# Kernel tuning notes

Hardware: AMD Instinct MI355X
Metric: run time of the kernel (lower is better)

The kernel has to match this reference:

```python
import jax, jax.numpy as jnp
import numpy as np

N_NODES = 10000
N_EDGES = 320000


def _graph_conv(x, W, b, src, dst, n):
    # DGL GraphConv, norm='both': D_out^{-1/2} on src side, aggregate, D_in^{-1/2} on dst side,
    # then linear + bias. Degrees clamped at 1 (allow_zero_in_degree=True).
    ones = jnp.ones(src.shape[0], dtype=x.dtype)
    deg_out = jnp.clip(jax.ops.segment_sum(ones, src, num_segments=n), 1.0)
    deg_in = jnp.clip(jax.ops.segment_sum(ones, dst, num_segments=n), 1.0)
    h = x * jax.lax.rsqrt(deg_out)[:, None]          # [n, f] scaled source feats
    agg = jax.ops.segment_sum(h[src], dst, num_segments=n)  # gather + scatter-add
    agg = agg * jax.lax.rsqrt(deg_in)[:, None]
    return agg @ W + b


def setup_inputs() -> dict:
    key = jax.random.key(0)
    ks = jax.random.split(key, 8)
    in_dim, h1, h2 = 512, 256, 128
    features = jax.random.normal(ks[0], (N_NODES, in_dim), dtype=jnp.float32)
    src = jax.random.randint(ks[1], (N_EDGES,), 0, N_NODES)
    dst = jax.random.randint(ks[2], (N_EDGES,), 0, N_NODES)
    noise = jax.random.normal(ks[3], (N_NODES, h2), dtype=jnp.float32)
    W1 = jax.random.normal(ks[4], (in_dim, h1), dtype=jnp.float32) / np.sqrt(in_dim)
    b1 = jnp.zeros((h1,), dtype=jnp.float32)
    W2 = jax.random.normal(ks[5], (h1, h2), dtype=jnp.float32) / np.sqrt(h1)
    b2 = jnp.zeros((h2,), dtype=jnp.float32)
    W3 = jax.random.normal(ks[6], (h1, h2), dtype=jnp.float32) / np.sqrt(h1)
    b3 = jnp.zeros((h2,), dtype=jnp.float32)
    return {"features": features, "src": src, "dst": dst, "noise": noise,
            "W1": W1, "b1": b1, "W2": W2, "b2": b2, "W3": W3, "b3": b3}


def reference(features, src, dst, noise, W1, b1, W2, b2, W3, b3):
    n = features.shape[0]
    h = jax.nn.relu(_graph_conv(features, W1, b1, src, dst, n))
    mean = _graph_conv(h, W2, b2, src, dst, n)
    log_std = _graph_conv(h, W3, b3, src, dst, n)
    z = mean + noise * jnp.exp(log_std)              # reparameterization
    adj_rec = jax.nn.sigmoid(z @ z.T)                # inner-product decoder [N, N]
    return adj_rec
```

## Files before the change

kernel.cpp:

```cpp
#include <hip/hip_runtime.h>
#include <hip/hip_fp16.h>


#define NN 10000
#define NE 320000
#define FD 512
#define H1 256
#define H2 128

typedef _Float16 half8 __attribute__((ext_vector_type(8)));
typedef _Float16 half4 __attribute__((ext_vector_type(4)));
typedef float f32x4 __attribute__((ext_vector_type(4)));

__device__ __forceinline__ void acc4(float4& a, const float4 v) {
    a.x += v.x; a.y += v.y; a.z += v.z; a.w += v.w;
}

__global__ void k_zero2(int* __restrict__ a, int* __restrict__ b, int n) {
    int i = blockIdx.x * blockDim.x + threadIdx.x;
    if (i < n) { a[i] = 0; b[i] = 0; }
}

__global__ void k_count(const int* __restrict__ src, const int* __restrict__ dst,
                        int* __restrict__ co, int* __restrict__ ci) {
    int e = blockIdx.x * blockDim.x + threadIdx.x;
    if (e < NE) {
        atomicAdd(&co[src[e]], 1);
        atomicAdd(&ci[dst[e]], 1);
    }
}

__global__ __launch_bounds__(1024) void k_scan(const int* __restrict__ ci, const int* __restrict__ co,
                                               int* __restrict__ row_ptr, int* __restrict__ cursor,
                                               float* __restrict__ rs_in, float* __restrict__ rs_out) {
    __shared__ int sm[1024];
    int tid = threadIdx.x;
    const int CH = (NN + 1023) / 1024;
    int base = tid * CH;
    int local[CH];
    int s = 0;
    #pragma unroll
    for (int i = 0; i < CH; ++i) {
        int idx = base + i;
        local[i] = s;
        if (idx < NN) s += ci[idx];
    }
    sm[tid] = s;
    __syncthreads();
    for (int off = 1; off < 1024; off <<= 1) {
        int v = (tid >= off) ? sm[tid - off] : 0;
        __syncthreads();
        sm[tid] += v;
        __syncthreads();
    }
    int excl = sm[tid] - s;
    #pragma unroll
    for (int i = 0; i < CH; ++i) {
        int idx = base + i;
        if (idx < NN) row_ptr[idx] = excl + local[i];
    }
    if (tid == 1023) row_ptr[NN] = sm[1023];
    for (int i = tid; i < NN; i += 1024) {
        int a = ci[i], b = co[i];
        rs_in[i]  = rsqrtf((float)(a > 1 ? a : 1));
        rs_out[i] = rsqrtf((float)(b > 1 ? b : 1));
        cursor[i] = 0;
    }
}

__global__ void k_bucket(const int* __restrict__ src, const int* __restrict__ dst,
                         const int* __restrict__ row_ptr, int* __restrict__ cursor,
                         int* __restrict__ esrc) {
    int e = blockIdx.x * blockDim.x + threadIdx.x;
    if (e < NE) {
        int d = dst[e];
        int p = row_ptr[d] + atomicAdd(&cursor[d], 1);
        esrc[p] = src[e];
    }
}

__global__ void k_castW(const float* __restrict__ W1, const float* __restrict__ W2,
                        const float* __restrict__ W3, const float* __restrict__ b2,
                        const float* __restrict__ b3,
                        _Float16* __restrict__ W1Th, _Float16* __restrict__ W1Tl,
                        _Float16* __restrict__ WcTh, _Float16* __restrict__ WcTl,
                        float* __restrict__ biasC) {
    int idx = blockIdx.x * blockDim.x + threadIdx.x;
    if (idx < FD * H1) {
        int k = idx >> 8, n = idx & 255;
        float v = W1[idx];
        _Float16 h = (_Float16)v;
        W1Th[n * FD + k] = h;
        W1Tl[n * FD + k] = (_Float16)(v - (float)h);
    } else if (idx < FD * H1 + H1 * H1) {
        int j = idx - FD * H1;
        int k = j >> 8, n = j & 255;
        float v = (n < H2) ? W2[k * H2 + n] : W3[k * H2 + (n - H2)];
        _Float16 h = (_Float16)v;
        WcTh[n * H1 + k] = h;
        WcTl[n * H1 + k] = (_Float16)(v - (float)h);
        if (k == 0) biasC[n] = (n < H2) ? b2[n] : b3[n - H2];
    }
}

template <int K>
__global__ __launch_bounds__(256) void k_gemm16(
    const float* __restrict__ A, const float* __restrict__ ascale,
    const _Float16* __restrict__ BTh, const _Float16* __restrict__ BTl,
    const float* __restrict__ bias, float* __restrict__ C, int M) {
    __shared__ __align__(16) _Float16 Ahs[64][72];
    __shared__ __align__(16) _Float16 Als[64][72];
    __shared__ __align__(16) _Float16 Bhs[64][72];
    __shared__ __align__(16) _Float16 Bls[64][72];
    int tid = threadIdx.x;
    int lane = tid & 63;
    int w = tid >> 6;
    int wr = (w >> 1) * 32, wc = (w & 1) * 32;
    int bm = blockIdx.x * 64, bn = blockIdx.y * 64;
    f32x4 acc[2][2] = {};
    for (int k0 = 0; k0 < K; k0 += 64) {
        __syncthreads();
        #pragma unroll
        for (int i = 0; i < 4; ++i) {
            int lin = i * 256 + tid;
            int r = lin >> 4, c = lin & 15;
            int gr = bm + r;
            float4 v = {0.f, 0.f, 0.f, 0.f};
            float s = 1.0f;
            if (gr < M) {
                v = *(const float4*)(A + (size_t)gr * K + k0 + c * 4);
                if (ascale) s = ascale[gr];
            }
            v.x *= s; v.y *= s; v.z *= s; v.w *= s;
            half4 hh = { (_Float16)v.x, (_Float16)v.y, (_Float16)v.z, (_Float16)v.w };
            half4 ll = { (_Float16)(v.x - (float)hh.x), (_Float16)(v.y - (float)hh.y),
                         (_Float16)(v.z - (float)hh.z), (_Float16)(v.w - (float)hh.w) };
            *(half4*)&Ahs[r][c * 4] = hh;
            *(half4*)&Als[r][c * 4] = ll;
        }
        #pragma unroll
        for (int i = 0; i < 2; ++i) {
            int lin = i * 256 + tid;
            int r = lin >> 3, c = lin & 7;
            *(int4*)&Bhs[r][c * 8] = *(const int4*)(BTh + (size_t)(bn + r) * K + k0 + c * 8);
            *(int4*)&Bls[r][c * 8] = *(const int4*)(BTl + (size_t)(bn + r) * K + k0 + c * 8);
        }
        __syncthreads();
        #pragma unroll
        for (int ks = 0; ks < 2; ++ks) {
            int kof = ks * 32 + ((lane >> 4) << 3);
            half8 ah[2], al[2], bh[2], bl[2];
            #pragma unroll
            for (int f = 0; f < 2; ++f) {
                ah[f] = *(const half8*)&Ahs[wr + f * 16 + (lane & 15)][kof];
                al[f] = *(const half8*)&Als[wr + f * 16 + (lane & 15)][kof];
                bh[f] = *(const half8*)&Bhs[wc + f * 16 + (lane & 15)][kof];
                bl[f] = *(const half8*)&Bls[wc + f * 16 + (lane & 15)][kof];
            }
            #pragma unroll
            for (int i = 0; i < 2; ++i)
                #pragma unroll
                for (int j = 0; j < 2; ++j) {
                    acc[i][j] = __builtin_amdgcn_mfma_f32_16x16x32_f16(ah[i], bh[j], acc[i][j], 0, 0, 0);
                    acc[i][j] = __builtin_amdgcn_mfma_f32_16x16x32_f16(ah[i], bl[j], acc[i][j], 0, 0, 0);
                    acc[i][j] = __builtin_amdgcn_mfma_f32_16x16x32_f16(al[i], bh[j], acc[i][j], 0, 0, 0);
                }
        }
    }
    int quad = lane >> 4, c16 = lane & 15;
    #pragma unroll
    for (int i = 0; i < 2; ++i) {
        int row0 = bm + wr + i * 16 + quad * 4;
        #pragma unroll
        for (int j = 0; j < 2; ++j) {
            int col = bn + wc + j * 16 + c16;
            float bb = bias ? bias[col] : 0.0f;
            #pragma unroll
            for (int r = 0; r < 4; ++r) {
                int row = row0 + r;
                if (row < M) C[(size_t)row * H1 + col] = acc[i][j][r] + bb;
            }
        }
    }
}

template <bool FIRST>
__global__ __launch_bounds__(256) void k_agg(const float* __restrict__ in, float* __restrict__ out,
                                             const int* __restrict__ esrc, const int* __restrict__ row_ptr,
                                             const float* __restrict__ rs_in, const float* __restrict__ rs_out,
                                             const float* __restrict__ bias) {
    int node = (blockIdx.x * blockDim.x + threadIdx.x) >> 6;
    int lane = threadIdx.x & 63;
    if (node >= NN) return;
    int beg = row_ptr[node], end = row_ptr[node + 1];
    float4 acc = {0.f, 0.f, 0.f, 0.f};
    int e = beg;
    for (; e + 4 <= end; e += 4) {
        int s0 = esrc[e + 0], s1 = esrc[e + 1], s2 = esrc[e + 2], s3 = esrc[e + 3];
        float4 v0 = ((const float4*)(in + (size_t)s0 * H1))[lane];
        float4 v1 = ((const float4*)(in + (size_t)s1 * H1))[lane];
        float4 v2 = ((const float4*)(in + (size_t)s2 * H1))[lane];
        float4 v3 = ((const float4*)(in + (size_t)s3 * H1))[lane];
        acc4(acc, v0); acc4(acc, v1); acc4(acc, v2); acc4(acc, v3);
    }
    for (; e < end; ++e) {
        float4 v0 = ((const float4*)(in + (size_t)esrc[e] * H1))[lane];
        acc4(acc, v0);
    }
    float si = rs_in[node];
    float4 r;
    r.x = acc.x * si; r.y = acc.y * si; r.z = acc.z * si; r.w = acc.w * si;
    if (FIRST) {
        float4 bb = ((const float4*)bias)[lane];
        float so = rs_out[node];
        r.x = fmaxf(r.x + bb.x, 0.f) * so;
        r.y = fmaxf(r.y + bb.y, 0.f) * so;
        r.z = fmaxf(r.z + bb.z, 0.f) * so;
        r.w = fmaxf(r.w + bb.w, 0.f) * so;
    }
    ((float4*)(out + (size_t)node * H1))[lane] = r;
}

__global__ void k_z(const float* __restrict__ ml, const float* __restrict__ noise,
                    _Float16* __restrict__ z) {
    int i = blockIdx.x * blockDim.x + threadIdx.x;
    if (i < NN * H2) {
        int r = i >> 7, c = i & 127;
        float mean = ml[(size_t)r * 256 + c];
        float ls   = ml[(size_t)r * 256 + 128 + c];
        z[i] = (_Float16)(mean + noise[i] * __expf(ls));
    }
}

__global__ __launch_bounds__(256) void k_decoder(const _Float16* __restrict__ Z, float* __restrict__ out) {
    __shared__ __align__(16) _Float16 As[128][72];
    __shared__ __align__(16) _Float16 Bs[128][72];
    int tid = threadIdx.x;
    int lane = tid & 63;
    int w = tid >> 6;
    int wrow = (w >> 1) * 64;
    int wcol = (w & 1) * 64;
    int rowBase = blockIdx.y * 128;
    int colBase = blockIdx.x * 128;
    f32x4 acc[4][4] = {};
    for (int s = 0; s < 2; ++s) {
        __syncthreads();
        #pragma unroll
        for (int i = 0; i < 4; ++i) {
            int lin = i * 256 + tid;
            int r = lin >> 3, c = lin & 7;
            int4 v = {0, 0, 0, 0};
            int gr = rowBase + r;
            if (gr < NN) v = *(const int4*)(Z + (size_t)gr * H2 + s * 64 + c * 8);
            *(int4*)&As[r][c * 8] = v;
            int4 u = {0, 0, 0, 0};
            int gc = colBase + r;
            if (gc < NN) u = *(const int4*)(Z + (size_t)gc * H2 + s * 64 + c * 8);
            *(int4*)&Bs[r][c * 8] = u;
        }
        __syncthreads();
        #pragma unroll
        for (int kk = 0; kk < 2; ++kk) {
            int kof = kk * 32 + ((lane >> 4) << 3);
            half8 a[4], b[4];
            #pragma unroll
            for (int f = 0; f < 4; ++f) a[f] = *(const half8*)&As[wrow + f * 16 + (lane & 15)][kof];
            #pragma unroll
            for (int f = 0; f < 4; ++f) b[f] = *(const half8*)&Bs[wcol + f * 16 + (lane & 15)][kof];
            #pragma unroll
            for (int i = 0; i < 4; ++i)
                #pragma unroll
                for (int j = 0; j < 4; ++j)
                    acc[i][j] = __builtin_amdgcn_mfma_f32_16x16x32_f16(a[i], b[j], acc[i][j], 0, 0, 0);
        }
    }
    #pragma unroll
    for (int i = 0; i < 4; ++i) {
        int row0 = rowBase + wrow + i * 16 + ((lane >> 4) << 2);
        #pragma unroll
        for (int j = 0; j < 4; ++j) {
            int col = colBase + wcol + j * 16 + (lane & 15);
            if (col < NN) {
                #pragma unroll
                for (int r = 0; r < 4; ++r) {
                    int row = row0 + r;
                    if (row < NN) {
                        float x = acc[i][j][r];
                        float sg = 1.0f / (1.0f + __expf(-x));
                        __builtin_nontemporal_store(sg, out + (size_t)row * NN + col);
                    }
                }
            }
        }
    }
}

extern "C" void kernel_launch(void* const* d_in, const int* in_sizes, int n_in,
                              void* d_out, int out_size, void* d_ws, size_t ws_size,
                              hipStream_t stream) {
    const float* features = (const float*)d_in[0];
    const int*   src      = (const int*)d_in[1];
    const int*   dst      = (const int*)d_in[2];
    const float* noise    = (const float*)d_in[3];
    const float* W1 = (const float*)d_in[4];
    const float* b1 = (const float*)d_in[5];
    const float* W2 = (const float*)d_in[6];
    const float* b2 = (const float*)d_in[7];
    const float* W3 = (const float*)d_in[8];
    const float* b3 = (const float*)d_in[9];
    float* out = (float*)d_out;
    (void)in_sizes; (void)n_in; (void)out_size; (void)ws_size;

    char* ws = (char*)d_ws;
    size_t off = 0;
    auto alloc = [&](size_t bytes) -> void* {
        void* p = ws + off;
        off += (bytes + 255) & ~(size_t)255;
        return p;
    };
    int* degc_out = (int*)alloc(NN * sizeof(int));
    int* degc_in  = (int*)alloc(NN * sizeof(int));
    int* row_ptr  = (int*)alloc((NN + 1) * sizeof(int));
    int* cursor   = (int*)alloc(NN * sizeof(int));
    int* esrc     = (int*)alloc(NE * sizeof(int));
    float* rs_out = (float*)alloc(NN * sizeof(float));
    float* rs_in  = (float*)alloc(NN * sizeof(float));
    _Float16* W1Th = (_Float16*)alloc((size_t)H1 * FD * sizeof(_Float16));
    _Float16* W1Tl = (_Float16*)alloc((size_t)H1 * FD * sizeof(_Float16));
    _Float16* WcTh = (_Float16*)alloc((size_t)H1 * H1 * sizeof(_Float16));
    _Float16* WcTl = (_Float16*)alloc((size_t)H1 * H1 * sizeof(_Float16));
    float* biasC  = (float*)alloc(H1 * sizeof(float));
    float* bufA   = (float*)alloc((size_t)NN * H1 * sizeof(float));
    float* bufB   = (float*)alloc((size_t)NN * H1 * sizeof(float));
    _Float16* Zh  = (_Float16*)alloc((size_t)NN * H2 * sizeof(_Float16));

    k_zero2<<<(NN + 255) / 256, 256, 0, stream>>>(degc_out, degc_in, NN);
    k_count<<<(NE + 255) / 256, 256, 0, stream>>>(src, dst, degc_out, degc_in);
    k_scan<<<1, 1024, 0, stream>>>(degc_in, degc_out, row_ptr, cursor, rs_in, rs_out);
    k_bucket<<<(NE + 255) / 256, 256, 0, stream>>>(src, dst, row_ptr, cursor, esrc);
    k_castW<<<(FD * H1 + H1 * H1 + 255) / 256, 256, 0, stream>>>(
        W1, W2, W3, b2, b3, W1Th, W1Tl, WcTh, WcTl, biasC);

    k_gemm16<FD><<<dim3((NN + 63) / 64, H1 / 64), 256, 0, stream>>>(
        features, rs_out, W1Th, W1Tl, nullptr, bufA, NN);
    k_agg<true><<<NN / 4, 256, 0, stream>>>(bufA, bufB, esrc, row_ptr, rs_in, rs_out, b1);
    k_agg<false><<<NN / 4, 256, 0, stream>>>(bufB, bufA, esrc, row_ptr, rs_in, nullptr, nullptr);
    k_gemm16<H1><<<dim3((NN + 63) / 64, H1 / 64), 256, 0, stream>>>(
        bufA, nullptr, WcTh, WcTl, biasC, bufB, NN);
    k_z<<<(NN * H2 + 255) / 256, 256, 0, stream>>>(bufB, noise, Zh);
    k_decoder<<<dim3((NN + 127) / 128, (NN + 127) / 128), 256, 0, stream>>>(Zh, out);
}
```

Measured before the change: 660.7 us.

## Store intermediate features as fp16 and fuse reparameterization into second GEMM

The first GEMM output and the post-ReLU hidden features are now stored as fp16, so the two gather-heavy aggregation kernels read half the bytes per edge. The second GEMM is restructured to compute matching mean and log_std column tiles in one block and apply bias, exp and the noise combination in its epilogue. This removes the separate k_z kernel and the fp32 round trip of the combined output. Smaller tweaks fold the cursor zeroing into the zero kernel and use a hardware reciprocal in the sigmoid. The fp16 storage of intermediates adds rounding error relative to the previous split-fp16 fp32 path.

Result: faster. 625.6 us (-5.3%).

```diff
diff --git a/kernel.cpp b/kernel.cpp
--- a/kernel.cpp
+++ b/kernel.cpp
@@ -12,13 +12,9 @@
 typedef _Float16 half4 __attribute__((ext_vector_type(4)));
 typedef float f32x4 __attribute__((ext_vector_type(4)));
 
-__device__ __forceinline__ void acc4(float4& a, const float4 v) {
-    a.x += v.x; a.y += v.y; a.z += v.z; a.w += v.w;
-}
-
-__global__ void k_zero2(int* __restrict__ a, int* __restrict__ b, int n) {
+__global__ void k_zero3(int* __restrict__ a, int* __restrict__ b, int* __restrict__ c, int n) {
     int i = blockIdx.x * blockDim.x + threadIdx.x;
-    if (i < n) { a[i] = 0; b[i] = 0; }
+    if (i < n) { a[i] = 0; b[i] = 0; c[i] = 0; }
 }
 
 __global__ void k_count(const int* __restrict__ src, const int* __restrict__ dst,
@@ -31,7 +27,7 @@
 }
 
 __global__ __launch_bounds__(1024) void k_scan(const int* __restrict__ ci, const int* __restrict__ co,
-                                               int* __restrict__ row_ptr, int* __restrict__ cursor,
+                                               int* __restrict__ row_ptr,
                                                float* __restrict__ rs_in, float* __restrict__ rs_out) {
     __shared__ int sm[1024];
     int tid = threadIdx.x;
@@ -64,7 +60,6 @@
         int a = ci[i], b = co[i];
         rs_in[i]  = rsqrtf((float)(a > 1 ? a : 1));
         rs_out[i] = rsqrtf((float)(b > 1 ? b : 1));
-        cursor[i] = 0;
     }
 }
 
@@ -80,11 +75,9 @@
 }
 
 __global__ void k_castW(const float* __restrict__ W1, const float* __restrict__ W2,
-                        const float* __restrict__ W3, const float* __restrict__ b2,
-                        const float* __restrict__ b3,
+                        const float* __restrict__ W3,
                         _Float16* __restrict__ W1Th, _Float16* __restrict__ W1Tl,
-                        _Float16* __restrict__ WcTh, _Float16* __restrict__ WcTl,
-                        float* __restrict__ biasC) {
+                        _Float16* __restrict__ WcTh, _Float16* __restrict__ WcTl) {
     int idx = blockIdx.x * blockDim.x + threadIdx.x;
     if (idx < FD * H1) {
         int k = idx >> 8, n = idx & 255;
@@ -99,15 +92,14 @@
         _Float16 h = (_Float16)v;
         WcTh[n * H1 + k] = h;
         WcTl[n * H1 + k] = (_Float16)(v - (float)h);
-        if (k == 0) biasC[n] = (n < H2) ? b2[n] : b3[n - H2];
-    }
-}
-
-template <int K>
-__global__ __launch_bounds__(256) void k_gemm16(
+    }
+}
+
+__global__ __launch_bounds__(256) void k_gemm1(
     const float* __restrict__ A, const float* __restrict__ ascale,
     const _Float16* __restrict__ BTh, const _Float16* __restrict__ BTl,
-    const float* __restrict__ bias, float* __restrict__ C, int M) {
+    _Float16* __restrict__ C, int M) {
+    const int K = FD;
     __shared__ __align__(16) _Float16 Ahs[64][72];
     __shared__ __align__(16) _Float16 Als[64][72];
     __shared__ __align__(16) _Float16 Bhs[64][72];
@@ -129,12 +121,12 @@
             float s = 1.0f;
             if (gr < M) {
                 v = *(const float4*)(A + (size_t)gr * K + k0 + c * 4);
-                if (ascale) s = ascale[gr];
+                s = ascale[gr];
             }
             v.x *= s; v.y *= s; v.z *= s; v.w *= s;
             half4 hh = { (_Float16)v.x, (_Float16)v.y, (_Float16)v.z, (_Float16)v.w };
-            half4 ll = { (_Float16)(v.x - (float)hh.x), (_Float16)(v.y - (float)hh.y),
-                         (_Float16)(v.z - (float)hh.z), (_Float16)(v.w - (float)hh.w) };
+            half4 ll = { (_Float16)(v.x - (float)hh[0]), (_Float16)(v.y - (float)hh[1]),
+                         (_Float16)(v.z - (float)hh[2]), (_Float16)(v.w - (float)hh[3]) };
             *(half4*)&Ahs[r][c * 4] = hh;
             *(half4*)&Als[r][c * 4] = ll;
         }
@@ -174,18 +166,113 @@
         #pragma unroll
         for (int j = 0; j < 2; ++j) {
             int col = bn + wc + j * 16 + c16;
-            float bb = bias ? bias[col] : 0.0f;
             #pragma unroll
             for (int r = 0; r < 4; ++r) {
                 int row = row0 + r;
-                if (row < M) C[(size_t)row * H1 + col] = acc[i][j][r] + bb;
+                if (row < M) C[(size_t)row * H1 + col] = (_Float16)acc[i][j][r];
+            }
+        }
+    }
+}
+
+__global__ __launch_bounds__(256) void k_gemm2z(
+    const float* __restrict__ A,
+    const _Float16* __restrict__ BTh, const _Float16* __restrict__ BTl,
+    const float* __restrict__ b2, const float* __restrict__ b3,
+    const float* __restrict__ noise, _Float16* __restrict__ Zh, int M) {
+    const int K = H1;
+    __shared__ __align__(16) _Float16 Ahs[64][72];
+    __shared__ __align__(16) _Float16 Als[64][72];
+    __shared__ __align__(16) _Float16 Bmh[64][72];
+    __shared__ __align__(16) _Float16 Bml[64][72];
+    __shared__ __align__(16) _Float16 Blh[64][72];
+    __shared__ __align__(16) _Float16 Bll[64][72];
+    int tid = threadIdx.x;
+    int lane = tid & 63;
+    int w = tid >> 6;
+    int wr = (w >> 1) * 32, wc = (w & 1) * 32;
+    int bm = blockIdx.x * 64;
+    int c0 = blockIdx.y * 64;
+    f32x4 accm[2][2] = {};
+    f32x4 accl[2][2] = {};
+    for (int k0 = 0; k0 < K; k0 += 64) {
+        __syncthreads();
+        #pragma unroll
+        for (int i = 0; i < 4; ++i) {
+            int lin = i * 256 + tid;
+            int r = lin >> 4, c = lin & 15;
+            int gr = bm + r;
+            float4 v = {0.f, 0.f, 0.f, 0.f};
+            if (gr < M) v = *(const float4*)(A + (size_t)gr * K + k0 + c * 4);
+            half4 hh = { (_Float16)v.x, (_Float16)v.y, (_Float16)v.z, (_Float16)v.w };
+            half4 ll = { (_Float16)(v.x - (float)hh[0]), (_Float16)(v.y - (float)hh[1]),
+                         (_Float16)(v.z - (float)hh[2]), (_Float16)(v.w - (float)hh[3]) };
+            *(half4*)&Ahs[r][c * 4] = hh;
+            *(half4*)&Als[r][c * 4] = ll;
+        }
+        #pragma unroll
+        for (int i = 0; i < 2; ++i) {
+            int lin = i * 256 + tid;
+            int r = lin >> 3, c = lin & 7;
+            size_t rm = (size_t)(c0 + r) * K + k0 + c * 8;
+            size_t rl = (size_t)(128 + c0 + r) * K + k0 + c * 8;
+            *(int4*)&Bmh[r][c * 8] = *(const int4*)(BTh + rm);
+            *(int4*)&Bml[r][c * 8] = *(const int4*)(BTl + rm);
+            *(int4*)&Blh[r][c * 8] = *(const int4*)(BTh + rl);
+            *(int4*)&Bll[r][c * 8] = *(const int4*)(BTl + rl);
+        }
+        __syncthreads();
+        #pragma unroll
+        for (int ks = 0; ks < 2; ++ks) {
+            int kof = ks * 32 + ((lane >> 4) << 3);
+            half8 ah[2], al[2], mh[2], ml[2], lh[2], ll[2];
+            #pragma unroll
+            for (int f = 0; f < 2; ++f) {
+                ah[f] = *(const half8*)&Ahs[wr + f * 16 + (lane & 15)][kof];
+                al[f] = *(const half8*)&Als[wr + f * 16 + (lane & 15)][kof];
+                mh[f] = *(const half8*)&Bmh[wc + f * 16 + (lane & 15)][kof];
+                ml[f] = *(const half8*)&Bml[wc + f * 16 + (lane & 15)][kof];
+                lh[f] = *(const half8*)&Blh[wc + f * 16 + (lane & 15)][kof];
+                ll[f] = *(const half8*)&Bll[wc + f * 16 + (lane & 15)][kof];
+            }
+            #pragma unroll
+            for (int i = 0; i < 2; ++i)
+                #pragma unroll
+                for (int j = 0; j < 2; ++j) {
+                    accm[i][j] = __builtin_amdgcn_mfma_f32_16x16x32_f16(ah[i], mh[j], accm[i][j], 0, 0, 0);
+                    accm[i][j] = __builtin_amdgcn_mfma_f32_16x16x32_f16(ah[i], ml[j], accm[i][j], 0, 0, 0);
+                    accm[i][j] = __builtin_amdgcn_mfma_f32_16x16x32_f16(al[i], mh[j], accm[i][j], 0, 0, 0);
+                    accl[i][j] = __builtin_amdgcn_mfma_f32_16x16x32_f16(ah[i], lh[j], accl[i][j], 0, 0, 0);
+                    accl[i][j] = __builtin_amdgcn_mfma_f32_16x16x32_f16(ah[i], ll[j], accl[i][j], 0, 0, 0);
+                    accl[i][j] = __builtin_amdgcn_mfma_f32_16x16x32_f16(al[i], lh[j], accl[i][j], 0, 0, 0);
+                }
+        }
+    }
+    int quad = lane >> 4, c16 = lane & 15;
+    #pragma unroll
+    for (int i = 0; i < 2; ++i) {
+        int row0 = bm + wr + i * 16 + quad * 4;
+        #pragma unroll
+        for (int j = 0; j < 2; ++j) {
+            int c = c0 + wc + j * 16 + c16;
+            float bm_ = b2[c], bl_ = b3[c];
+            #pragma unroll
+            for (int r = 0; r < 4; ++r) {
+                int row = row0 + r;
+                if (row < M) {
+                    float mean = accm[i][j][r] + bm_;
+                    float lsv  = accl[i][j][r] + bl_;
+                    float z = mean + noise[(size_t)row * H2 + c] * __expf(lsv);
+                    Zh[(size_t)row * H2 + c] = (_Float16)z;
+                }
             }
         }
     }
 }
 
 template <bool FIRST>
-__global__ __launch_bounds__(256) void k_agg(const float* __restrict__ in, float* __restrict__ out,
+__global__ __launch_bounds__(256) void k_agg(const _Float16* __restrict__ in,
+                                             _Float16* __restrict__ outh, float* __restrict__ outf,
                                              const int* __restrict__ esrc, const int* __restrict__ row_ptr,
                                              const float* __restrict__ rs_in, const float* __restrict__ rs_out,
                                              const float* __restrict__ bias) {
@@ -193,42 +280,37 @@
     int lane = threadIdx.x & 63;
     if (node >= NN) return;
     int beg = row_ptr[node], end = row_ptr[node + 1];
-    float4 acc = {0.f, 0.f, 0.f, 0.f};
+    float a0 = 0.f, a1 = 0.f, a2 = 0.f, a3 = 0.f;
     int e = beg;
     for (; e + 4 <= end; e += 4) {
         int s0 = esrc[e + 0], s1 = esrc[e + 1], s2 = esrc[e + 2], s3 = esrc[e + 3];
-        float4 v0 = ((const float4*)(in + (size_t)s0 * H1))[lane];
-        float4 v1 = ((const float4*)(in + (size_t)s1 * H1))[lane];
-        float4 v2 = ((const float4*)(in + (size_t)s2 * H1))[lane];
-        float4 v3 = ((const float4*)(in + (size_t)s3 * H1))[lane];
-        acc4(acc, v0); acc4(acc, v1); acc4(acc, v2); acc4(acc, v3);
+        half4 v0 = ((const half4*)(in + (size_t)s0 * H1))[lane];
+        half4 v1 = ((const half4*)(in + (size_t)s1 * H1))[lane];
+        half4 v2 = ((const half4*)(in + (size_t)s2 * H1))[lane];
+        half4 v3 = ((const half4*)(in + (size_t)s3 * H1))[lane];
+        a0 += (float)v0[0] + (float)v1[0] + (float)v2[0] + (float)v3[0];
+        a1 += (float)v0[1] + (float)v1[1] + (float)v2[1] + (float)v3[1];
+        a2 += (float)v0[2] + (float)v1[2] + (float)v2[2] + (float)v3[2];
+        a3 += (float)v0[3] + (float)v1[3] + (float)v2[3] + (float)v3[3];
     }
     for (; e < end; ++e) {
-        float4 v0 = ((const float4*)(in + (size_t)esrc[e] * H1))[lane];
-        acc4(acc, v0);
+        half4 v0 = ((const half4*)(in + (size_t)esrc[e] * H1))[lane];
+        a0 += (float)v0[0]; a1 += (float)v0[1]; a2 += (float)v0[2]; a3 += (float)v0[3];
     }
     float si = rs_in[node];
-    float4 r;
-    r.x = acc.x * si; r.y = acc.y * si; r.z = acc.z * si; r.w = acc.w * si;
+    a0 *= si; a1 *= si; a2 *= si; a3 *= si;
     if (FIRST) {
         float4 bb = ((const float4*)bias)[lane];
         float so = rs_out[node];
-        r.x = fmaxf(r.x + bb.x, 0.f) * so;
-        r.y = fmaxf(r.y + bb.y, 0.f) * so;
-        r.z = fmaxf(r.z + bb.z, 0.f) * so;
-        r.w = fmaxf(r.w + bb.w, 0.f) * so;
-    }
-    ((float4*)(out + (size_t)node * H1))[lane] = r;
-}
-
-__global__ void k_z(const float* __restrict__ ml, const float* __restrict__ noise,
-                    _Float16* __restrict__ z) {
-    int i = blockIdx.x * blockDim.x + threadIdx.x;
-    if (i < NN * H2) {
-        int r = i >> 7, c = i & 127;
-        float mean = ml[(size_t)r * 256 + c];
-        float ls   = ml[(size_t)r * 256 + 128 + c];
-        z[i] = (_Float16)(mean + noise[i] * __expf(ls));
+        a0 = fmaxf(a0 + bb.x, 0.f) * so;
+        a1 = fmaxf(a1 + bb.y, 0.f) * so;
+        a2 = fmaxf(a2 + bb.z, 0.f) * so;
+        a3 = fmaxf(a3 + bb.w, 0.f) * so;
+        half4 hh = { (_Float16)a0, (_Float16)a1, (_Float16)a2, (_Float16)a3 };
+        ((half4*)(outh + (size_t)node * H1))[lane] = hh;
+    } else {
+        float4 r = { a0, a1, a2, a3 };
+        ((float4*)(outf + (size_t)node * H1))[lane] = r;
     }
 }
 
@@ -286,7 +368,7 @@
                     int row = row0 + r;
                     if (row < NN) {
                         float x = acc[i][j][r];
-                        float sg = 1.0f / (1.0f + __expf(-x));
+                        float sg = __builtin_amdgcn_rcpf(1.0f + __expf(-x));
                         __builtin_nontemporal_store(sg, out + (size_t)row * NN + col);
                     }
                 }
@@ -329,24 +411,23 @@
     _Float16* W1Tl = (_Float16*)alloc((size_t)H1 * FD * sizeof(_Float16));
     _Float16* WcTh = (_Float16*)alloc((size_t)H1 * H1 * sizeof(_Float16));
     _Float16* WcTl = (_Float16*)alloc((size_t)H1 * H1 * sizeof(_Float16));
-    float* biasC  = (float*)alloc(H1 * sizeof(float));
-    float* bufA   = (float*)alloc((size_t)NN * H1 * sizeof(float));
-    float* bufB   = (float*)alloc((size_t)NN * H1 * sizeof(float));
-    _Float16* Zh  = (_Float16*)alloc((size_t)NN * H2 * sizeof(_Float16));
-
-    k_zero2<<<(NN + 255) / 256, 256, 0, stream>>>(degc_out, degc_in, NN);
+    _Float16* y1h  = (_Float16*)alloc((size_t)NN * H1 * sizeof(_Float16));
+    _Float16* hh   = (_Float16*)alloc((size_t)NN * H1 * sizeof(_Float16));
+    float* agg2    = (float*)alloc((size_t)NN * H1 * sizeof(float));
+    _Float16* Zh   = (_Float16*)alloc((size_t)NN * H2 * sizeof(_Float16));
+
+    k_zero3<<<(NN + 255) / 256, 256, 0, stream>>>(degc_out, degc_in, cursor, NN);
     k_count<<<(NE + 255) / 256, 256, 0, stream>>>(src, dst, degc_out, degc_in);
-    k_scan<<<1, 1024, 0, stream>>>(degc_in, degc_out, row_ptr, cursor, rs_in, rs_out);
+    k_scan<<<1, 1024, 0, stream>>>(degc_in, degc_out, row_ptr, rs_in, rs_out);
     k_bucket<<<(NE + 255) / 256, 256, 0, stream>>>(src, dst, row_ptr, cursor, esrc);
     k_castW<<<(FD * H1 + H1 * H1 + 255) / 256, 256, 0, stream>>>(
-        W1, W2, W3, b2, b3, W1Th, W1Tl, WcTh, WcTl, biasC);
-
-    k_gemm16<FD><<<dim3((NN + 63) / 64, H1 / 64), 256, 0, stream>>>(
-        features, rs_out, W1Th, W1Tl, nullptr, bufA, NN);
-    k_agg<true><<<NN / 4, 256, 0, stream>>>(bufA, bufB, esrc, row_ptr, rs_in, rs_out, b1);
-    k_agg<false><<<NN / 4, 256, 0, stream>>>(bufB, bufA, esrc, row_ptr, rs_in, nullptr, nullptr);
-    k_gemm16<H1><<<dim3((NN + 63) / 64, H1 / 64), 256, 0, stream>>>(
-        bufA, nullptr, WcTh, WcTl, biasC, bufB, NN);
-    k_z<<<(NN * H2 + 255) / 256, 256, 0, stream>>>(bufB, noise, Zh);
+        W1, W2, W3, W1Th, W1Tl, WcTh, WcTl);
+
+    k_gemm1<<<dim3((NN + 63) / 64, H1 / 64), 256, 0, stream>>>(
+        features, rs_out, W1Th, W1Tl, y1h, NN);
+    k_agg<true><<<NN / 4, 256, 0, stream>>>(y1h, hh, nullptr, esrc, row_ptr, rs_in, rs_out, b1);
+    k_agg<false><<<NN / 4, 256, 0, stream>>>(hh, nullptr, agg2, esrc, row_ptr, rs_in, nullptr, nullptr);
+    k_gemm2z<<<dim3((NN + 63) / 64, H2 / 64), 256, 0, stream>>>(
+        agg2, WcTh, WcTl, b2, b3, noise, Zh, NN);
     k_decoder<<<dim3((NN + 127) / 128, (NN + 127) / 128), 256, 0, stream>>>(Zh, out);
 }
```
